# Optimization experiments

Hardware: AMD Instinct MI355X
Metric: run time of the kernel (lower is better)

Reference implementation:

```python
import jax, jax.numpy as jnp
import numpy as np

L_SEG = 20   # number of CFT segments (hard-coded in original forward)
M_CHEB = 8   # Chebyshev quadrature order per segment


def _cft_magnitude(x, modes):
    """|CFT(x)| at integer frequencies [0, modes).

    Faithful to vectorized_batched_cft_decomposed with L=20, M=8, but only
    evaluated at the first `modes` frequencies (identical values; the original
    computes all rfft freqs then slices). Segment loop is folded into a single
    einsum by absorbing the per-segment phase shift into the quadrature weights.
    x: (B, C, N) real. Returns (B, C, modes) float.
    """
    n = x.shape[-1]
    t = jnp.linspace(0.0, 1.0, n)
    freqs = jnp.arange(modes, dtype=x.dtype)  # rfftfreq(n, d=1/n)[:modes]
    seg_len = 1.0 / L_SEG
    starts = jnp.linspace(0.0, 1.0, L_SEG + 1)[:-1]  # (L,)
    k = jnp.arange(M_CHEB, dtype=x.dtype)
    cheb = -jnp.cos((2.0 * k + 1.0) * jnp.pi / (2.0 * M_CHEB))  # (M,) nodes in [-1,1]
    T = jnp.cos(k[:, None] * jnp.arccos(cheb)[None, :])  # (K=M, M) Chebyshev T_k at nodes
    angle = cheb[:, None] * (freqs[None, :] * (2.0 * jnp.pi * seg_len / 2.0))  # (M, F)
    Wr = jnp.einsum('km,mf->kf', T, jnp.cos(angle)) * (seg_len / 2.0)  # (M, F)
    Wi = jnp.einsum('km,mf->kf', T, -jnp.sin(angle)) * (seg_len / 2.0)
    # piecewise-linear interpolation of x at the Chebyshev nodes of every segment
    t_seg = starts[:, None] + seg_len / 2.0 * (cheb + 1.0)[None, :]  # (L, M)
    right = jnp.clip(jnp.searchsorted(t, t_seg), 0, n - 1)
    left = jnp.clip(right - 1, 0, None)
    t_l, t_r = t[left], t[right]
    denom = jnp.where(t_r - t_l == 0.0, 1.0, t_r - t_l)
    w_r = (t_seg - t_l) / denom
    w_l = 1.0 - w_r
    seg = w_l * x[:, :, left] + w_r * x[:, :, right]  # (B, C, L, M)
    # per-segment phase shift exp(-i*2*pi*f*a) folded into combined weights
    phi = 2.0 * jnp.pi * starts[:, None] * freqs[None, :]  # (L, F)
    cs, sn = jnp.cos(phi), jnp.sin(phi)
    Ar = Wr[None] * cs[:, None, :] + Wi[None] * sn[:, None, :]   # (L, M, F)
    Ai = -Wr[None] * sn[:, None, :] + Wi[None] * cs[:, None, :]
    real = jnp.einsum('bclm,lmf->bcf', seg, Ar)
    imag = jnp.einsum('bclm,lmf->bcf', seg, Ai)
    return jnp.sqrt(real * real + imag * imag)


def setup_inputs() -> dict:
    key = jax.random.key(0)
    ks = jax.random.split(key, 4)
    B, Cin, Cout, N, modes = 32, 64, 64, 8192, 32
    scale = 1.0 / (Cin * Cout)
    return {
        'x': jax.random.normal(ks[0], (B, Cin, N), dtype=jnp.float32),
        'w1_real': scale * jax.random.uniform(ks[1], (Cin, Cout, modes), dtype=jnp.float32),
        'w1_imag': scale * jax.random.uniform(ks[2], (Cin, Cout, modes), dtype=jnp.float32),
        'gate_w': jax.random.normal(ks[3], (Cout, Cin), dtype=jnp.float32) / np.sqrt(Cin),
        'ln_gamma': jnp.ones((modes,), dtype=jnp.float32),
        'ln_beta': jnp.zeros((modes,), dtype=jnp.float32),
    }


def reference(x, w1_real, w1_imag, gate_w, ln_gamma, ln_beta):
    n = x.shape[-1]
    n_rfft = n // 2 + 1
    modes = w1_real.shape[-1]
    x_fft = jnp.fft.rfft(x)  # (B, C, n_rfft) complex64
    # CFT magnitude is detached in the original (x_cft.detach())
    mag = jax.lax.stop_gradient(_cft_magnitude(x, modes))  # (B, C, modes)
    # LayerNorm over the modes axis (eps = 1e-5, torch default)
    mu = jnp.mean(mag, axis=-1, keepdims=True)
    var = jnp.mean((mag - mu) ** 2, axis=-1, keepdims=True)
    g_norm = (mag - mu) / jnp.sqrt(var + 1e-5) * ln_gamma + ln_beta
    # 1x1 conv (no bias) over channels, then sigmoid gate
    gate = jax.nn.sigmoid(jnp.einsum('oi,bif->bof', gate_w, g_norm))  # (B, Cout, modes)
    gated = x_fft[:, :, :modes] * gate  # requires Cin == Cout
    w1 = w1_real + 1j * w1_imag  # (Cin, Cout, modes) complex
    out_modes = jnp.einsum('bix,iox->box', gated, w1)
    pad = jnp.zeros(out_modes.shape[:2] + (n_rfft - modes,), dtype=out_modes.dtype)
    out_ft = jnp.concatenate([out_modes, pad], axis=-1)
    return jnp.fft.irfft(out_ft, n=n)
```

## Files before the change

kernel.cpp:

```cpp
#include <hip/hip_runtime.h>
#include <hip/hip_bf16.h>
#include <math.h>

#define NN    8192
#define NROWS 2048
#define FF    32
#define LM    160

static constexpr int TRIG   = 0;
static constexpr int W1RT   = 524288;
static constexpr int W1IT   = 655360;
static constexpr int GWT    = 786432;
static constexpr int AR_    = 790528;
static constexpr int AI_    = 795648;
static constexpr int WL_    = 800768;
static constexpr int WR_    = 800928;
static constexpr int IL_    = 801088;
static constexpr int IR_    = 801248;
static constexpr int XR_    = 801408;
static constexpr int XI_    = 866944;
static constexpr int GN_    = 932480;
static constexpr int ARAI   = 998016;
static constexpr int TRIGT_ = 1129088;

#define PI_D 3.14159265358979323846

__global__ __launch_bounds__(256) void k_trig(float* __restrict__ ws) {
  int idx = blockIdx.x * 256 + threadIdx.x;
  int k4 = idx >> 8, f = (idx >> 2) & 63, j = idx & 3;
  int n = 4 * k4 + j;
  int fr = f & 31;
  int p = (fr * n) & (NN - 1);
  float ang = (float)p * (float)(2.0 * PI_D / (double)NN);
  float s, c;
  sincosf(ang, &s, &c);
  float v = (f < 32) ? c : s;
  ws[TRIG + idx] = v;
  ws[TRIGT_ + f * NN + n] = v;
}

__global__ __launch_bounds__(256) void k_cft_tables(float* __restrict__ ws) {
  int tid = blockIdx.x * 256 + threadIdx.x;
  if (tid >= LM * FF) return;
  int j = tid >> 5, f = tid & 31;
  int l = j >> 3, m = j & 7;
  double cheb[8];
  #pragma unroll
  for (int mm = 0; mm < 8; ++mm)
    cheb[mm] = -cos((2.0 * mm + 1.0) * PI_D / 16.0);

  double Wr = 0.0, Wi = 0.0;
  #pragma unroll
  for (int mm = 0; mm < 8; ++mm) {
    double T = cos((double)m * acos(cheb[mm]));
    double ang = cheb[mm] * (double)f * (PI_D * 0.05);
    Wr += T * cos(ang);
    Wi += T * (-sin(ang));
  }
  Wr *= 0.025; Wi *= 0.025;
  double phi = 2.0 * PI_D * ((double)l * 0.05) * (double)f;
  double cs = cos(phi), sn = sin(phi);
  ws[AR_ + j * FF + f] = (float)(Wr * cs + Wi * sn);
  ws[AI_ + j * FF + f] = (float)(-Wr * sn + Wi * cs);

  if (f == 0) {
    double v = (double)l * 0.05 + 0.025 * (cheb[m] + 1.0);
    int r = (int)(v * 8191.0);
    while ((double)r / 8191.0 < v) ++r;
    while (r > 0 && (double)(r - 1) / 8191.0 >= v) --r;
    if (r > 8191) r = 8191;
    int le = r - 1; if (le < 0) le = 0;
    double tl = (double)le / 8191.0, tr = (double)r / 8191.0;
    double den = (tr - tl == 0.0) ? 1.0 : (tr - tl);
    double wr = (v - tl) / den;
    ws[WL_ + j] = (float)(1.0 - wr);
    ws[WR_ + j] = (float)wr;
    ((int*)ws)[IL_ + j] = le;
    ((int*)ws)[IR_ + j] = r;
  }
}

__global__ __launch_bounds__(256) void k_transpose(const float* __restrict__ w1r,
                                                   const float* __restrict__ w1i,
                                                   const float* __restrict__ gw,
                                                   float* __restrict__ ws) {
  int idx = blockIdx.x * 256 + threadIdx.x;
  if (idx >= 32 * 64 * 64) return;
  int o = idx & 63, i = (idx >> 6) & 63, f = idx >> 12;
  ws[W1RT + (f * 64 + i) * 64 + o] = w1r[(i * 64 + o) * FF + f];
  ws[W1IT + (f * 64 + i) * 64 + o] = w1i[(i * 64 + o) * FF + f];
  if (idx < 4096) {
    ws[GWT + idx] = gw[(idx & 63) * 64 + (idx >> 6)];
  }
}

__global__ __launch_bounds__(256) void k_fwd_gemm(const float* __restrict__ x,
                                                  const float* __restrict__ ws,
                                                  float* __restrict__ part) {
  __shared__ __align__(16) float xs[64 * 128];
  const int rt = blockIdx.x >> 6, kc = blockIdx.x & 63;
  const int t = threadIdx.x;
  const int w = t >> 6, lane = t & 63;
  const int half = lane >> 5, fl = lane & 31;
  const int rblock = rt * 64;
  const float4* __restrict__ tg4 = (const float4*)(ws + TRIG);
  const int k40 = kc * 32;

  float4 tc = tg4[(size_t)k40 * 64 + fl];
  float4 tn = tg4[(size_t)k40 * 64 + 32 + fl];

  const int c4 = t & 31, r0 = t >> 5;
  const int kb = kc * 128;
  #pragma unroll
  for (int p = 0; p < 8; ++p) {
    int row = r0 + 8 * p;
    float4 v = *(const float4*)(x + (size_t)(rblock + row) * NN + kb + c4 * 4);
    *(float4*)(&xs[row * 128 + c4 * 4]) = v;
  }

  float accC[8], accS[8];
  #pragma unroll
  for (int r = 0; r < 8; ++r) { accC[r] = 0.f; accS[r] = 0.f; }

  __syncthreads();

  const float* __restrict__ xbase = &xs[(w * 16 + half * 8) * 128];

#define FWD_STEP(IT, TC, TS)                                                    \
  {                                                                             \
    _Pragma("unroll")                                                           \
    for (int j = 0; j < 8; ++j) {                                               \
      float4 xv = *(const float4*)(xbase + j * 128 + (IT) * 4);                 \
      accC[j] = fmaf(xv.w, (TC).w, fmaf(xv.z, (TC).z,                           \
                fmaf(xv.y, (TC).y, fmaf(xv.x, (TC).x, accC[j]))));              \
      accS[j] = fmaf(xv.w, (TS).w, fmaf(xv.z, (TS).z,                           \
                fmaf(xv.y, (TS).y, fmaf(xv.x, (TS).x, accS[j]))));              \
    }                                                                           \
  }

  #pragma unroll 4
  for (int it = 0; it < 31; ++it) {
    float4 tc2 = tg4[(size_t)(k40 + it + 1) * 64 + fl];
    float4 tn2 = tg4[(size_t)(k40 + it + 1) * 64 + 32 + fl];
    FWD_STEP(it, tc, tn);
    tc = tc2; tn = tn2;
  }
  FWD_STEP(31, tc, tn);
#undef FWD_STEP

  float* __restrict__ pp = part + ((size_t)kc * NROWS + rblock + w * 16 + half * 8) * 64;
  #pragma unroll
  for (int j = 0; j < 8; ++j) {
    pp[j * 64 + fl]      = accC[j];
    pp[j * 64 + 32 + fl] = accS[j];
  }
}

__global__ __launch_bounds__(256) void k_fred(const float* __restrict__ part,
                                              float* __restrict__ ws) {
  int idx = blockIdx.x * 256 + threadIdx.x;
  int row = idx >> 6, f = idx & 63;
  float s = 0.f;
  #pragma unroll 8
  for (int kc = 0; kc < 64; ++kc)
    s += part[((size_t)kc * NROWS + row) * 64 + f];
  if (f < 32) ws[XR_ + row * FF + f] = s;
  else        ws[XI_ + row * FF + (f - 32)] = -s;
}

__global__ __launch_bounds__(256) void k_cft(const float* __restrict__ x,
                                             const float* __restrict__ gamma,
                                             const float* __restrict__ beta,
                                             float* __restrict__ ws) {
  const int sub = threadIdx.x >> 6, li = threadIdx.x & 63;
  const int row = blockIdx.x * 4 + sub;
  const float* __restrict__ xr = x + (size_t)row * NN;
  __shared__ float seg[4][LM];
  #pragma unroll
  for (int g = 0; g < 3; ++g) {
    int j = li + 64 * g;
    if (j < LM) {
      int il = ((const int*)ws)[IL_ + j];
      int ir = ((const int*)ws)[IR_ + j];
      seg[sub][j] = ws[WL_ + j] * xr[il] + ws[WR_ + j] * xr[ir];
    }
  }
  __syncthreads();
  if (li < FF) {
    float re = 0.f, im = 0.f;
    #pragma unroll 8
    for (int j = 0; j < LM; ++j) {
      float sv = seg[sub][j];
      re = fmaf(sv, ws[AR_ + j * FF + li], re);
      im = fmaf(sv, ws[AI_ + j * FF + li], im);
    }
    float mag = sqrtf(re * re + im * im);
    float mu = mag;
    mu += __shfl_xor(mu, 1);  mu += __shfl_xor(mu, 2);  mu += __shfl_xor(mu, 4);
    mu += __shfl_xor(mu, 8);  mu += __shfl_xor(mu, 16);
    mu *= (1.0f / 32.0f);
    float d = mag - mu;
    float vv = d * d;
    vv += __shfl_xor(vv, 1);  vv += __shfl_xor(vv, 2);  vv += __shfl_xor(vv, 4);
    vv += __shfl_xor(vv, 8);  vv += __shfl_xor(vv, 16);
    vv *= (1.0f / 32.0f);
    float g = d / sqrtf(vv + 1e-5f) * gamma[li] + beta[li];
    ws[GN_ + row * FF + li] = g;
  }
}

__global__ __launch_bounds__(64) void k_gate(float* __restrict__ ws) {
  int bidx = blockIdx.x;
  int b = bidx >> 5, f = bidx & 31;
  int o = threadIdx.x;
  __shared__ float gn[64], gr[64], gi[64];
  int rowb = b * 64;
  gn[o] = ws[GN_ + (rowb + o) * FF + f];
  float xre = ws[XR_ + (rowb + o) * FF + f];
  float xim = ws[XI_ + (rowb + o) * FF + f];
  __syncthreads();
  float acc = 0.f;
  #pragma unroll 16
  for (int i = 0; i < 64; ++i)
    acc = fmaf(ws[GWT + i * 64 + o], gn[i], acc);
  float gate = 1.0f / (1.0f + expf(-acc));
  gr[o] = xre * gate;
  gi[o] = xim * gate;
  __syncthreads();
  float Yr = 0.f, Yi = 0.f;
  const float* __restrict__ w1rt = ws + W1RT + f * 4096;
  const float* __restrict__ w1it = ws + W1IT + f * 4096;
  #pragma unroll 8
  for (int i = 0; i < 64; ++i) {
    float a = gr[i], bb2 = gi[i];
    float wr = w1rt[i * 64 + o], wi = w1it[i * 64 + o];
    Yr = fmaf(a, wr, Yr); Yr = fmaf(-bb2, wi, Yr);
    Yi = fmaf(a, wi, Yi); Yi = fmaf(bb2, wr, Yi);
  }
  float* A = ws + ARAI + (size_t)(rowb + o) * 64;
  if (f == 0) {
    A[0]  = Yr * (1.0f / (float)NN);
    A[32] = 0.0f;
  } else {
    A[f]      = Yr * (2.0f / (float)NN);
    A[32 + f] = -Yi * (2.0f / (float)NN);
  }
}

__global__ __launch_bounds__(256) void k_inv(const float* __restrict__ ws,
                                             float* __restrict__ out) {
  __shared__ __align__(16) float As[32 * 64];
  const int blk = blockIdx.x;
  const int bb = blk >> 5, cc = blk & 31;
  const int t = threadIdx.x;
  const int w = t >> 6, lane = t & 63;
  const int rowbase = bb * 32;
  const float* __restrict__ trigt = ws + TRIGT_;
  const int colb = cc * 256 + lane * 4;

  float4 tg0 = *(const float4*)(trigt + (size_t)0 * NN + colb);
  float4 tg1 = *(const float4*)(trigt + (size_t)1 * NN + colb);
  float4 tg2 = *(const float4*)(trigt + (size_t)2 * NN + colb);
  float4 tg3 = *(const float4*)(trigt + (size_t)3 * NN + colb);

  #pragma unroll
  for (int p = 0; p < 2; ++p) {
    int idx = t + 256 * p;
    int r = idx >> 4, q = idx & 15;
    *(float4*)(&As[r * 64 + q * 4]) =
        *(const float4*)(ws + ARAI + (size_t)(rowbase + r) * 64 + q * 4);
  }

  float4 acc[8];
  #pragma unroll
  for (int r = 0; r < 8; ++r) acc[r] = make_float4(0.f, 0.f, 0.f, 0.f);

  __syncthreads();

#define INV_STEP(F0)                                                            \
  {                                                                             \
    _Pragma("unroll")                                                           \
    for (int r = 0; r < 8; ++r) {                                               \
      float4 av = *(const float4*)(&As[(w * 8 + r) * 64 + (F0)]);               \
      acc[r].x = fmaf(av.x, tg0.x, acc[r].x); acc[r].y = fmaf(av.x, tg0.y, acc[r].y); \
      acc[r].z = fmaf(av.x, tg0.z, acc[r].z); acc[r].w = fmaf(av.x, tg0.w, acc[r].w); \
      acc[r].x = fmaf(av.y, tg1.x, acc[r].x); acc[r].y = fmaf(av.y, tg1.y, acc[r].y); \
      acc[r].z = fmaf(av.y, tg1.z, acc[r].z); acc[r].w = fmaf(av.y, tg1.w, acc[r].w); \
      acc[r].x = fmaf(av.z, tg2.x, acc[r].x); acc[r].y = fmaf(av.z, tg2.y, acc[r].y); \
      acc[r].z = fmaf(av.z, tg2.z, acc[r].z); acc[r].w = fmaf(av.z, tg2.w, acc[r].w); \
      acc[r].x = fmaf(av.w, tg3.x, acc[r].x); acc[r].y = fmaf(av.w, tg3.y, acc[r].y); \
      acc[r].z = fmaf(av.w, tg3.z, acc[r].z); acc[r].w = fmaf(av.w, tg3.w, acc[r].w); \
    }                                                                           \
  }

  for (int fo = 0; fo < 15; ++fo) {
    int f0 = fo * 4;
    float4 n0 = *(const float4*)(trigt + (size_t)(f0 + 4) * NN + colb);
    float4 n1 = *(const float4*)(trigt + (size_t)(f0 + 5) * NN + colb);
    float4 n2 = *(const float4*)(trigt + (size_t)(f0 + 6) * NN + colb);
    float4 n3 = *(const float4*)(trigt + (size_t)(f0 + 7) * NN + colb);
    INV_STEP(f0);
    tg0 = n0; tg1 = n1; tg2 = n2; tg3 = n3;
  }
  INV_STEP(60);
#undef INV_STEP

  #pragma unroll
  for (int r = 0; r < 8; ++r) {
    int row = rowbase + w * 8 + r;
    *(float4*)(out + (size_t)row * NN + colb) = acc[r];
  }
}

extern "C" void kernel_launch(void* const* d_in, const int* in_sizes, int n_in,
                              void* d_out, int out_size, void* d_ws, size_t ws_size,
                              hipStream_t stream) {
  const float* x     = (const float*)d_in[0];
  const float* w1r   = (const float*)d_in[1];
  const float* w1i   = (const float*)d_in[2];
  const float* gw    = (const float*)d_in[3];
  const float* gamma = (const float*)d_in[4];
  const float* beta  = (const float*)d_in[5];
  float* out = (float*)d_out;
  float* ws = (float*)d_ws;
  float* part = (float*)d_out;

  hipLaunchKernelGGL(k_trig,       dim3(2048), dim3(256), 0, stream, ws);
  hipLaunchKernelGGL(k_cft_tables, dim3(20),   dim3(256), 0, stream, ws);
  hipLaunchKernelGGL(k_transpose,  dim3(512),  dim3(256), 0, stream, w1r, w1i, gw, ws);
  hipLaunchKernelGGL(k_fwd_gemm,   dim3(2048), dim3(256), 0, stream, x, ws, part);
  hipLaunchKernelGGL(k_fred,       dim3(512),  dim3(256), 0, stream, part, ws);
  hipLaunchKernelGGL(k_cft,        dim3(512),  dim3(256), 0, stream, x, gamma, beta, ws);
  hipLaunchKernelGGL(k_gate,       dim3(1024), dim3(64),  0, stream, ws);
  hipLaunchKernelGGL(k_inv,        dim3(2048), dim3(256), 0, stream, ws, out);
}
```

Measured before the change: 211.1 us.

## Restructure forward DFT GEMM with async LDS double-buffering and fewer K partials

The forward DFT GEMM now uses 32-row tiles that each cover a 512-wide K chunk. It streams x into double-buffered LDS with global_load_lds, so the next slice loads while the current one is computed. The two half-waves split K and combine their results with a lane shuffle. This cuts the partial-sum buffer from 64 chunks to 16 and lets the reduction kernel use float4 loads, reducing partial write/read traffic. The cost is more syncs per block and a dependence on the async LDS load builtin, and each block now holds 32 KB of LDS.

```diff
diff --git a/kernel.cpp b/kernel.cpp
--- a/kernel.cpp
+++ b/kernel.cpp
@@ -25,6 +25,12 @@
 
 #define PI_D 3.14159265358979323846
 
+__device__ __forceinline__ void load_lds16(const float* g, float* l) {
+  __builtin_amdgcn_global_load_lds(
+      (const __attribute__((address_space(1))) void*)g,
+      (__attribute__((address_space(3))) void*)l, 16, 0, 0);
+}
+
 __global__ __launch_bounds__(256) void k_trig(float* __restrict__ ws) {
   int idx = blockIdx.x * 256 + threadIdx.x;
   int k4 = idx >> 8, f = (idx >> 2) & 63, j = idx & 3;
@@ -94,28 +100,26 @@
   }
 }
 
-__global__ __launch_bounds__(256) void k_fwd_gemm(const float* __restrict__ x,
-                                                  const float* __restrict__ ws,
-                                                  float* __restrict__ part) {
-  __shared__ __align__(16) float xs[64 * 128];
-  const int rt = blockIdx.x >> 6, kc = blockIdx.x & 63;
+__global__ __launch_bounds__(256, 4) void k_fwd_gemm(const float* __restrict__ x,
+                                                     const float* __restrict__ ws,
+                                                     float* __restrict__ part) {
+  __shared__ __align__(16) float xs[2][32 * 128];
+  const int rt = blockIdx.x >> 4, kg = blockIdx.x & 15;
   const int t = threadIdx.x;
   const int w = t >> 6, lane = t & 63;
   const int half = lane >> 5, fl = lane & 31;
-  const int rblock = rt * 64;
+  const int khalf = half * 16;
+  const int rblock = rt * 32;
   const float4* __restrict__ tg4 = (const float4*)(ws + TRIG);
-  const int k40 = kc * 32;
-
-  float4 tc = tg4[(size_t)k40 * 64 + fl];
-  float4 tn = tg4[(size_t)k40 * 64 + 32 + fl];
-
+  const int k40 = kg * 128;
+  const int kb  = kg * 512;
   const int c4 = t & 31, r0 = t >> 5;
-  const int kb = kc * 128;
-  #pragma unroll
-  for (int p = 0; p < 8; ++p) {
+
+  #pragma unroll
+  for (int p = 0; p < 4; ++p) {
     int row = r0 + 8 * p;
-    float4 v = *(const float4*)(x + (size_t)(rblock + row) * NN + kb + c4 * 4);
-    *(float4*)(&xs[row * 128 + c4 * 4]) = v;
+    load_lds16(x + (size_t)(rblock + row) * NN + kb + c4 * 4,
+               &xs[0][row * 128 + c4 * 4]);
   }
 
   float accC[8], accS[8];
@@ -124,48 +128,76 @@
 
   __syncthreads();
 
-  const float* __restrict__ xbase = &xs[(w * 16 + half * 8) * 128];
-
-#define FWD_STEP(IT, TC, TS)                                                    \
+#define FWD_STEP(COL, TC, TS)                                                   \
   {                                                                             \
+    float4 xv[8];                                                               \
+    _Pragma("unroll")                                                           \
+    for (int j = 0; j < 8; ++j)                                                 \
+      xv[j] = *(const float4*)(xbase + j * 128 + (COL) * 4);                    \
     _Pragma("unroll")                                                           \
     for (int j = 0; j < 8; ++j) {                                               \
-      float4 xv = *(const float4*)(xbase + j * 128 + (IT) * 4);                 \
-      accC[j] = fmaf(xv.w, (TC).w, fmaf(xv.z, (TC).z,                           \
-                fmaf(xv.y, (TC).y, fmaf(xv.x, (TC).x, accC[j]))));              \
-      accS[j] = fmaf(xv.w, (TS).w, fmaf(xv.z, (TS).z,                           \
-                fmaf(xv.y, (TS).y, fmaf(xv.x, (TS).x, accS[j]))));              \
+      accC[j] = fmaf(xv[j].w, (TC).w, fmaf(xv[j].z, (TC).z,                     \
+                fmaf(xv[j].y, (TC).y, fmaf(xv[j].x, (TC).x, accC[j]))));        \
+      accS[j] = fmaf(xv[j].w, (TS).w, fmaf(xv[j].z, (TS).z,                     \
+                fmaf(xv[j].y, (TS).y, fmaf(xv[j].x, (TS).x, accS[j]))));        \
     }                                                                           \
   }
 
-  #pragma unroll 4
-  for (int it = 0; it < 31; ++it) {
-    float4 tc2 = tg4[(size_t)(k40 + it + 1) * 64 + fl];
-    float4 tn2 = tg4[(size_t)(k40 + it + 1) * 64 + 32 + fl];
-    FWD_STEP(it, tc, tn);
-    tc = tc2; tn = tn2;
-  }
-  FWD_STEP(31, tc, tn);
+  for (int sc = 0; sc < 4; ++sc) {
+    if (sc < 3) {
+      #pragma unroll
+      for (int p = 0; p < 4; ++p) {
+        int row = r0 + 8 * p;
+        load_lds16(x + (size_t)(rblock + row) * NN + kb + (sc + 1) * 128 + c4 * 4,
+                   &xs[(sc + 1) & 1][row * 128 + c4 * 4]);
+      }
+    }
+    const float* __restrict__ xbase = &xs[sc & 1][w * 8 * 128];
+    const int gbase = k40 + sc * 32 + khalf;
+    float4 tc = tg4[(size_t)gbase * 64 + fl];
+    float4 tn = tg4[(size_t)gbase * 64 + 32 + fl];
+    #pragma unroll 5
+    for (int it = 0; it < 15; ++it) {
+      float4 tc2 = tg4[(size_t)(gbase + it + 1) * 64 + fl];
+      float4 tn2 = tg4[(size_t)(gbase + it + 1) * 64 + 32 + fl];
+      FWD_STEP(khalf + it, tc, tn);
+      tc = tc2; tn = tn2;
+    }
+    FWD_STEP(khalf + 15, tc, tn);
+    __syncthreads();
+  }
 #undef FWD_STEP
 
-  float* __restrict__ pp = part + ((size_t)kc * NROWS + rblock + w * 16 + half * 8) * 64;
   #pragma unroll
   for (int j = 0; j < 8; ++j) {
-    pp[j * 64 + fl]      = accC[j];
-    pp[j * 64 + 32 + fl] = accS[j];
-  }
+    accC[j] += __shfl_xor(accC[j], 32);
+    accS[j] += __shfl_xor(accS[j], 32);
+  }
+
+  const int coloff = khalf * 2 + fl;
+  float* __restrict__ pp = part + ((size_t)kg * NROWS + rblock + w * 8) * 64;
+  #pragma unroll
+  for (int j = 0; j < 8; ++j)
+    pp[j * 64 + coloff] = half ? accS[j] : accC[j];
 }
 
 __global__ __launch_bounds__(256) void k_fred(const float* __restrict__ part,
                                               float* __restrict__ ws) {
   int idx = blockIdx.x * 256 + threadIdx.x;
-  int row = idx >> 6, f = idx & 63;
-  float s = 0.f;
-  #pragma unroll 8
-  for (int kc = 0; kc < 64; ++kc)
-    s += part[((size_t)kc * NROWS + row) * 64 + f];
-  if (f < 32) ws[XR_ + row * FF + f] = s;
-  else        ws[XI_ + row * FF + (f - 32)] = -s;
+  int row = idx >> 4, fq = idx & 15;
+  const float4* __restrict__ p4 = (const float4*)part;
+  float4 s = make_float4(0.f, 0.f, 0.f, 0.f);
+  #pragma unroll
+  for (int kc = 0; kc < 16; ++kc) {
+    float4 v = p4[((size_t)kc * NROWS + row) * 16 + fq];
+    s.x += v.x; s.y += v.y; s.z += v.z; s.w += v.w;
+  }
+  if (fq < 8) {
+    *(float4*)(ws + XR_ + row * FF + fq * 4) = s;
+  } else {
+    float4 n = make_float4(-s.x, -s.y, -s.z, -s.w);
+    *(float4*)(ws + XI_ + row * FF + (fq - 8) * 4) = n;
+  }
 }
 
 __global__ __launch_bounds__(256) void k_cft(const float* __restrict__ x,
@@ -328,8 +360,8 @@
   hipLaunchKernelGGL(k_trig,       dim3(2048), dim3(256), 0, stream, ws);
   hipLaunchKernelGGL(k_cft_tables, dim3(20),   dim3(256), 0, stream, ws);
   hipLaunchKernelGGL(k_transpose,  dim3(512),  dim3(256), 0, stream, w1r, w1i, gw, ws);
-  hipLaunchKernelGGL(k_fwd_gemm,   dim3(2048), dim3(256), 0, stream, x, ws, part);
-  hipLaunchKernelGGL(k_fred,       dim3(512),  dim3(256), 0, stream, part, ws);
+  hipLaunchKernelGGL(k_fwd_gemm,   dim3(1024), dim3(256), 0, stream, x, ws, part);
+  hipLaunchKernelGGL(k_fred,       dim3(128),  dim3(256), 0, stream, part, ws);
   hipLaunchKernelGGL(k_cft,        dim3(512),  dim3(256), 0, stream, x, gamma, beta, ws);
   hipLaunchKernelGGL(k_gate,       dim3(1024), dim3(64),  0, stream, ws);
   hipLaunchKernelGGL(k_inv,        dim3(2048), dim3(256), 0, stream, ws, out);
```

Measured after the change: 222.1 us. 1.05x slower.
